# Kernel optimization log

Measured on AMD Instinct MI355X. Metric: run time of the kernel, lower is better.

## Reference

```python
import jax, jax.numpy as jnp
import numpy as np

N_NODES = 100000
N_EDGES = 1200000
NUM_GRAPHS = 128
IN_DIM = 5
HIDDEN = 64


def setup_inputs() -> dict:
    key = jax.random.key(0)
    ks = jax.random.split(key, 12)
    x = jax.random.normal(ks[0], (N_NODES, IN_DIM), dtype=jnp.float32)
    edge_index = jax.random.randint(ks[1], (2, N_EDGES), 0, N_NODES, dtype=jnp.int64 if jax.config.read('jax_enable_x64') else jnp.int32)
    batch = jnp.sort(jax.random.randint(ks[2], (N_NODES,), 0, NUM_GRAPHS, dtype=jnp.int32))
    s = lambda fan_in: 1.0 / np.sqrt(fan_in)
    return {
        'x': x,
        'edge_index': edge_index,
        'batch': batch,
        'w_rel1': jax.random.normal(ks[3], (IN_DIM, HIDDEN), dtype=jnp.float32) * s(IN_DIM),
        'b_rel1': jnp.zeros((HIDDEN,), dtype=jnp.float32),
        'w_root1': jax.random.normal(ks[4], (IN_DIM, HIDDEN), dtype=jnp.float32) * s(IN_DIM),
        'w_rel2': jax.random.normal(ks[5], (HIDDEN, HIDDEN), dtype=jnp.float32) * s(HIDDEN),
        'b_rel2': jnp.zeros((HIDDEN,), dtype=jnp.float32),
        'w_root2': jax.random.normal(ks[6], (HIDDEN, HIDDEN), dtype=jnp.float32) * s(HIDDEN),
        'w_h1': jax.random.normal(ks[7], (2 * HIDDEN, HIDDEN), dtype=jnp.float32) * s(2 * HIDDEN),
        'b_h1': jnp.zeros((HIDDEN,), dtype=jnp.float32),
        'w_h2': jax.random.normal(ks[8], (HIDDEN, 1), dtype=jnp.float32) * s(HIDDEN),
        'b_h2': jnp.zeros((1,), dtype=jnp.float32),
    }


def _graph_conv(x, src, dst, w_rel, b_rel, w_root):
    # PyG GraphConv (aggr='add'): out = aggr(x_src -> dst) @ W_rel + b_rel + x @ W_root
    agg = jax.ops.segment_sum(x[src], dst, num_segments=N_NODES)
    return agg @ w_rel + b_rel + x @ w_root


def reference(x, edge_index, batch,
              w_rel1, b_rel1, w_root1,
              w_rel2, b_rel2, w_root2,
              w_h1, b_h1, w_h2, b_h2):
    src, dst = edge_index[0], edge_index[1]
    h = jax.nn.relu(_graph_conv(x, src, dst, w_rel1, b_rel1, w_root1))
    h = jax.nn.relu(_graph_conv(h, src, dst, w_rel2, b_rel2, w_root2))
    # global add + mean pooling over graphs
    add_pool = jax.ops.segment_sum(h, batch, num_segments=NUM_GRAPHS)
    counts = jax.ops.segment_sum(jnp.ones((N_NODES,), h.dtype), batch, num_segments=NUM_GRAPHS)
    mean_pool = add_pool / jnp.maximum(counts, 1.0)[:, None]
    g = jnp.concatenate([mean_pool, add_pool], axis=1)  # [G, 2*HIDDEN]
    out = jax.nn.relu(g @ w_h1 + b_h1) @ w_h2 + b_h2
    return out.squeeze(-1)
```

## Files before the change

### kernel.cpp

```cpp
#include <hip/hip_runtime.h>
#include <hip/hip_bf16.h>

#define N_NODES    100000
#define N_EDGES    1200000
#define NUM_GRAPHS 128
#define IN_DIM     5
#define HIDDEN     64
#define M_TILES    (N_NODES / 16)
#define NI4        (N_EDGES / 4)

#define CB    782
#define CBLK  256
#define EPB   ((NI4 + CBLK - 1) / CBLK)
#define STCAP 3072
#define AGP   72

typedef __attribute__((ext_vector_type(8))) short short8;
typedef __attribute__((ext_vector_type(4))) float f32x4;
typedef __attribute__((ext_vector_type(2))) float f32x2;

#if defined(__has_builtin)
#if __has_builtin(__builtin_amdgcn_cvt_pk_f32_fp8)
#define HAS_HWF8 1
#endif
#endif

__device__ __forceinline__ unsigned short f2bs(float f) {
    union { float f; unsigned u; } v; v.f = f;
    return (unsigned short)((v.u + 0x7FFFu + ((v.u >> 16) & 1u)) >> 16);
}
__device__ __forceinline__ float bs2f(unsigned short s) {
    union { unsigned u; float f; } v; v.u = ((unsigned)s) << 16;
    return v.f;
}
__device__ __forceinline__ float blo(unsigned p) { return bs2f((unsigned short)(p & 0xffff)); }
__device__ __forceinline__ float bhi(unsigned p) { return bs2f((unsigned short)(p >> 16)); }
__device__ __forceinline__ unsigned pack2(float a, float b) {
    return ((unsigned)f2bs(b) << 16) | (unsigned)f2bs(a);
}

__device__ __forceinline__ unsigned char f2f8(float f) {
    union { float f; unsigned u; } v; v.f = f * 0x1p-120f;
    unsigned u = v.u + 0x7FFFFu + ((v.u >> 20) & 1u);
    return (unsigned char)(u >> 20);
}
__device__ __forceinline__ float f82f(unsigned b) {
    union { unsigned u; float f; } v; v.u = (b & 0x7Fu) << 20;
    return v.f * 0x1p120f;
}

__device__ __forceinline__ void acc8(float4& a, unsigned r) {
#ifdef HAS_HWF8
    f32x2 lo = __builtin_amdgcn_cvt_pk_f32_fp8((int)r, false);
    f32x2 hi = __builtin_amdgcn_cvt_pk_f32_fp8((int)r, true);
    a.x += lo[0]; a.y += lo[1]; a.z += hi[0]; a.w += hi[1];
#else
    a.x += f82f(r); a.y += f82f(r >> 8); a.z += f82f(r >> 16); a.w += f82f(r >> 24);
#endif
}


__global__ void coarse_count(const int* __restrict__ dst, int* __restrict__ gcnt,
                             const float* __restrict__ x, uint4* __restrict__ xb,
                             float* __restrict__ add_pool, int* __restrict__ ptr) {
    __shared__ int h[CB];
    int t = threadIdx.x, b = blockIdx.x;
    for (int i = t; i < CB; i += 256) h[i] = 0;
    __syncthreads();
    int i0 = b * EPB, i1 = min(i0 + EPB, NI4);
    for (int i = i0 + t; i < i1; i += 256) {
        int4 d = ((const int4*)dst)[i];
        atomicAdd(&h[d.x >> 7], 1);
        atomicAdd(&h[d.y >> 7], 1);
        atomicAdd(&h[d.z >> 7], 1);
        atomicAdd(&h[d.w >> 7], 1);
    }
    __syncthreads();
    for (int i = t; i < CB; i += 256) gcnt[b * CB + i] = h[i];

    for (int n = b * 256 + t; n < N_NODES; n += CBLK * 256) {
        const float* xr = x + (size_t)n * IN_DIM;
        uint4 o;
        o.x = pack2(xr[0], xr[1]);
        o.y = pack2(xr[2], xr[3]);
        o.z = pack2(xr[4], 0.0f);
        o.w = 0u;
        xb[n] = o;
    }
    if (b == 0) {
        for (int i = t; i < NUM_GRAPHS * HIDDEN; i += 256) add_pool[i] = 0.0f;
        if (t == 0) ptr[N_NODES] = N_EDGES;
    }
}

__global__ void block_scan(int* __restrict__ gcnt, int* __restrict__ btot) {
    __shared__ int s[CBLK];
    int k = blockIdx.x, t = threadIdx.x;
    int v = gcnt[t * CB + k];
    s[t] = v;
    __syncthreads();
    for (int off = 1; off < CBLK; off <<= 1) {
        int u = (t >= off) ? s[t - off] : 0;
        __syncthreads();
        s[t] += u;
        __syncthreads();
    }
    gcnt[t * CB + k] = s[t] - v;
    if (t == CBLK - 1) btot[k] = s[t];
}

__global__ void partition_k(const int* __restrict__ src, const int* __restrict__ dst,
                            const int* __restrict__ gcnt, const int* __restrict__ btot,
                            int* __restrict__ bstart, int* __restrict__ part) {
    __shared__ int sb[CB];
    __shared__ int base[CB];
    __shared__ int h[CB];
    int t = threadIdx.x, b = blockIdx.x;
    for (int i = t; i < CB; i += 256) sb[i] = btot[i];
    __syncthreads();
    if (t < 64) {
        int loc[13];
        int base_i = t * 13;
        int sum = 0;
#pragma unroll
        for (int j = 0; j < 13; ++j) {
            int idx = base_i + j;
            int c = (idx < CB) ? sb[idx] : 0;
            loc[j] = sum; sum += c;
        }
        int inc = sum;
#pragma unroll
        for (int off = 1; off < 64; off <<= 1) {
            int u = __shfl_up(inc, off, 64);
            if (t >= off) inc += u;
        }
        int excl = inc - sum;
#pragma unroll
        for (int j = 0; j < 13; ++j) {
            int idx = base_i + j;
            if (idx < CB) sb[idx] = excl + loc[j];
        }
    }
    __syncthreads();
    for (int i = t; i < CB; i += 256) {
        int bs = sb[i];
        base[i] = bs + gcnt[b * CB + i];
        h[i] = 0;
        if (b == 0) bstart[i] = bs;
    }
    if (b == 0 && t == 0) bstart[CB] = N_EDGES;
    __syncthreads();
    int i0 = b * EPB, i1 = min(i0 + EPB, NI4);
    for (int i = i0 + t; i < i1; i += 256) {
        int4 s4 = ((const int4*)src)[i];
        int4 d4 = ((const int4*)dst)[i];
        int k, r;
        k = d4.x >> 7; r = atomicAdd(&h[k], 1); part[base[k] + r] = s4.x | ((d4.x & 127) << 17);
        k = d4.y >> 7; r = atomicAdd(&h[k], 1); part[base[k] + r] = s4.y | ((d4.y & 127) << 17);
        k = d4.z >> 7; r = atomicAdd(&h[k], 1); part[base[k] + r] = s4.z | ((d4.z & 127) << 17);
        k = d4.w >> 7; r = atomicAdd(&h[k], 1); part[base[k] + r] = s4.w | ((d4.w & 127) << 17);
    }
}

__global__ void fine_gather1(const int* __restrict__ part, const int* __restrict__ bstart,
                             int* __restrict__ ptr, int* __restrict__ esrc,
                             const uint4* __restrict__ xb,
                             const float* __restrict__ x,
                             const float* __restrict__ w_rel1,
                             const float* __restrict__ b_rel1,
                             const float* __restrict__ w_root1,
                             unsigned short* __restrict__ h1,
                             unsigned char* __restrict__ h1f8) {
    __shared__ int fh[128];
    __shared__ int fo[128];
    __shared__ int fr[128];
    __shared__ uint4 stage[STCAP];
    int k = blockIdx.x, t = threadIdx.x;
    int e0 = bstart[k], e1 = bstart[k + 1];
    int ne = e1 - e0;
    bool useLds = (ne <= STCAP);
    if (t < 128) { fh[t] = 0; fr[t] = 0; }
    __syncthreads();
    for (int e = e0 + t; e < e1; e += 256)
        atomicAdd(&fh[(part[e] >> 17) & 127], 1);
    __syncthreads();
    int v = (t < 128) ? fh[t] : 0;
    if (t < 128) fo[t] = v;
    __syncthreads();
    for (int off = 1; off < 128; off <<= 1) {
        int u = (t >= off && t < 128) ? fo[t - off] : 0;
        __syncthreads();
        if (t < 128) fo[t] += u;
        __syncthreads();
    }
    if (t < 128) {
        int excl = fo[t] - v;
        int n_t = (k << 7) + t;
        if (n_t < N_NODES) ptr[n_t] = e0 + excl;
        fh[t] = excl;
    }
    __syncthreads();
    for (int e = e0 + t; e < e1; e += 256) {
        int p = part[e];
        int d = (p >> 17) & 127;
        int s = p & 0x1FFFF;
        int r = atomicAdd(&fr[d], 1);
        int slot = fh[d] + r;
        esrc[e0 + slot] = s;
        if (useLds) stage[slot] = xb[s];
    }
    __syncthreads();

    int ql = t & 15;
    int g  = t >> 4;
    float wr[IN_DIM][4], wo[IN_DIM][4], bias[4];
#pragma unroll
    for (int j = 0; j < 4; ++j) {
        int ch = ql * 4 + j;
        bias[j] = b_rel1[ch];
#pragma unroll
        for (int kk = 0; kk < IN_DIM; ++kk) {
            wr[kk][j] = w_rel1[kk * HIDDEN + ch];
            wo[kk][j] = w_root1[kk * HIDDEN + ch];
        }
    }

    for (int nl = g; nl < 128; nl += 16) {
        int n = (k << 7) + nl;
        if (n >= N_NODES) break;
        int s0 = fh[nl];
        int s1 = (nl < 127) ? fh[nl + 1] : ne;
        float a[IN_DIM] = {0.f, 0.f, 0.f, 0.f, 0.f};
        if (useLds) {
            for (int i = s0 + ql; i < s1; i += 16) {
                uint4 p = stage[i];
                a[0] += blo(p.x); a[1] += bhi(p.x);
                a[2] += blo(p.y); a[3] += bhi(p.y);
                a[4] += blo(p.z);
            }
        } else {
            for (int i = s0 + ql; i < s1; i += 16) {
                uint4 p = xb[esrc[e0 + i]];
                a[0] += blo(p.x); a[1] += bhi(p.x);
                a[2] += blo(p.y); a[3] += bhi(p.y);
                a[4] += blo(p.z);
            }
        }
#pragma unroll
        for (int kk = 0; kk < IN_DIM; ++kk) {
            a[kk] += __shfl_xor(a[kk], 1, 64);
            a[kk] += __shfl_xor(a[kk], 2, 64);
            a[kk] += __shfl_xor(a[kk], 4, 64);
            a[kk] += __shfl_xor(a[kk], 8, 64);
        }
        float xr[IN_DIM];
#pragma unroll
        for (int kk = 0; kk < IN_DIM; ++kk) xr[kk] = x[(size_t)n * IN_DIM + kk];

        unsigned short hv[4];
        unsigned char  hf[4];
#pragma unroll
        for (int j = 0; j < 4; ++j) {
            float acc = bias[j];
#pragma unroll
            for (int kk = 0; kk < IN_DIM; ++kk)
                acc += a[kk] * wr[kk][j] + xr[kk] * wo[kk][j];
            float h = fmaxf(acc, 0.0f);
            hv[j] = f2bs(h);
            hf[j] = f2f8(h);
        }
        ushort4 v4; v4.x = hv[0]; v4.y = hv[1]; v4.z = hv[2]; v4.w = hv[3];
        *(ushort4*)(h1 + (size_t)n * HIDDEN + ql * 4) = v4;
        uchar4 c4; c4.x = hf[0]; c4.y = hf[1]; c4.z = hf[2]; c4.w = hf[3];
        *(uchar4*)(h1f8 + (size_t)n * HIDDEN + ql * 4) = c4;
    }
}

__global__ void gather2_mlp2(const unsigned* __restrict__ rows,
                             const int* __restrict__ ptr,
                             const int* __restrict__ esrc,
                             const unsigned short* __restrict__ h1,
                             const float* __restrict__ w_rel2,
                             const float* __restrict__ b_rel2,
                             const float* __restrict__ w_root2,
                             const int* __restrict__ batch,
                             float* __restrict__ add_pool) {
    __shared__ unsigned short ag[16 * AGP];
    int tid  = threadIdx.x;
    int lane = tid & 63, wv = tid >> 6;
    int row  = lane & 15, quad = lane >> 4;
    int n    = wv * 16 + row;
    int g    = tid >> 4, ql = tid & 15;

    short8 bwr[2], bwo[2];
#pragma unroll
    for (int s = 0; s < 2; ++s)
#pragma unroll
        for (int j = 0; j < 8; ++j) {
            int k = 32 * s + quad * 8 + j;
            bwr[s][j] = (short)f2bs(w_rel2[k * HIDDEN + n]);
            bwo[s][j] = (short)f2bs(w_root2[k * HIDDEN + n]);
        }
    float bias = b_rel2[n];

    for (int t = blockIdx.x; t < M_TILES; t += gridDim.x) {
        int m0 = t * 16;
        int nd = m0 + g;
        int start = ptr[nd], end = ptr[nd + 1];
        float4 a0 = {0.f, 0.f, 0.f, 0.f}, a1 = a0;
        int e = start;
        for (; e + 1 < end; e += 2) {
            int sA = esrc[e], sB = esrc[e + 1];
            unsigned r0 = rows[(size_t)sA * 16 + ql];
            unsigned r1 = rows[(size_t)sB * 16 + ql];
            acc8(a0, r0); acc8(a1, r1);
        }
        if (e < end) {
            unsigned r0 = rows[(size_t)esrc[e] * 16 + ql];
            acc8(a0, r0);
        }
        a0.x += a1.x; a0.y += a1.y; a0.z += a1.z; a0.w += a1.w;
        uint2 pk;
        pk.x = pack2(a0.x, a0.y);
        pk.y = pack2(a0.z, a0.w);
        *(uint2*)&ag[g * AGP + ql * 4] = pk;
        __syncthreads();

        size_t rbase = (size_t)(m0 + row) * HIDDEN;
        short8 aa0 = *(const short8*)&ag[row * AGP + quad * 8];
        short8 aa1 = *(const short8*)&ag[row * AGP + 32 + quad * 8];
        short8 ah0 = *(const short8*)(h1 + rbase + quad * 8);
        short8 ah1 = *(const short8*)(h1 + rbase + 32 + quad * 8);

        f32x4 acc = {bias, bias, bias, bias};
        acc = __builtin_amdgcn_mfma_f32_16x16x32_bf16(aa0, bwr[0], acc, 0, 0, 0);
        acc = __builtin_amdgcn_mfma_f32_16x16x32_bf16(aa1, bwr[1], acc, 0, 0, 0);
        acc = __builtin_amdgcn_mfma_f32_16x16x32_bf16(ah0, bwo[0], acc, 0, 0, 0);
        acc = __builtin_amdgcn_mfma_f32_16x16x32_bf16(ah1, bwo[1], acc, 0, 0, 0);

        float hv0 = fmaxf(acc[0], 0.0f), hv1 = fmaxf(acc[1], 0.0f);
        float hv2 = fmaxf(acc[2], 0.0f), hv3 = fmaxf(acc[3], 0.0f);

        int gLo = batch[m0], gHi = batch[m0 + 15];
        if (gLo == gHi) {
            float s = (hv0 + hv1) + (hv2 + hv3);
            s += __shfl_xor(s, 16, 64);
            s += __shfl_xor(s, 32, 64);
            if (quad == 0)
                atomicAdd(&add_pool[gLo * HIDDEN + n], s);
        } else {
            int m = m0 + quad * 4;
            atomicAdd(&add_pool[batch[m]     * HIDDEN + n], hv0);
            atomicAdd(&add_pool[batch[m + 1] * HIDDEN + n], hv1);
            atomicAdd(&add_pool[batch[m + 2] * HIDDEN + n], hv2);
            atomicAdd(&add_pool[batch[m + 3] * HIDDEN + n], hv3);
        }
        __syncthreads();
    }
}

__device__ __forceinline__ int lower_bound_i(const int* a, int n, int v) {
    int lo = 0, hi = n;
    while (lo < hi) { int mid = (lo + hi) >> 1; if (a[mid] < v) lo = mid + 1; else hi = mid; }
    return lo;
}

__global__ void head_mlp(const float* __restrict__ add_pool,
                         const int* __restrict__ batch,
                         const float* __restrict__ w_h1,
                         const float* __restrict__ b_h1,
                         const float* __restrict__ w_h2,
                         const float* __restrict__ b_h2,
                         float* __restrict__ out) {
    int g = blockIdx.x, t = threadIdx.x;

    __shared__ int s_cnt;
    if (t == 0) {
        int start = lower_bound_i(batch, N_NODES, g);
        int end   = lower_bound_i(batch, N_NODES, g + 1);
        s_cnt = end - start;
    }
    __syncthreads();
    float cnt = fmaxf((float)s_cnt, 1.0f);

    __shared__ float sg[2 * HIDDEN];
    float add = add_pool[(size_t)g * HIDDEN + t];
    sg[t]          = add / cnt;
    sg[HIDDEN + t] = add;
    __syncthreads();

    float hid = b_h1[t];
#pragma unroll 16
    for (int i = 0; i < 2 * HIDDEN; ++i)
        hid += sg[i] * w_h1[i * HIDDEN + t];
    hid = fmaxf(hid, 0.0f);

    float res = hid * w_h2[t];
    for (int off = 32; off > 0; off >>= 1)
        res += __shfl_down(res, off, 64);
    if (t == 0) out[g] = res + b_h2[0];
}

extern "C" void kernel_launch(void* const* d_in, const int* in_sizes, int n_in,
                              void* d_out, int out_size, void* d_ws, size_t ws_size,
                              hipStream_t stream) {
    const float* x       = (const float*)d_in[0];
    const int*   ei      = (const int*)d_in[1];
    const int*   src     = ei;
    const int*   dst     = ei + N_EDGES;
    const int*   batch   = (const int*)d_in[2];
    const float* w_rel1  = (const float*)d_in[3];
    const float* b_rel1  = (const float*)d_in[4];
    const float* w_root1 = (const float*)d_in[5];
    const float* w_rel2  = (const float*)d_in[6];
    const float* b_rel2  = (const float*)d_in[7];
    const float* w_root2 = (const float*)d_in[8];
    const float* w_h1    = (const float*)d_in[9];
    const float* b_h1    = (const float*)d_in[10];
    const float* w_h2    = (const float*)d_in[11];
    const float* b_h2    = (const float*)d_in[12];
    float* out = (float*)d_out;

    int* base = (int*)d_ws;
    int*   gcnt     = base;
    int*   btot     = gcnt + ((CBLK * CB + 3) & ~3);
    int*   bstart   = btot + ((CB + 3) & ~3);
    float* add_pool = (float*)(bstart + ((CB + 1 + 3) & ~3));
    int*   ptr      = (int*)(add_pool + NUM_GRAPHS * HIDDEN);
    int*   part     = ptr + ((N_NODES + 1 + 3) & ~3);
    int*   esrc     = part + N_EDGES;
    unsigned short* h1   = (unsigned short*)(esrc + N_EDGES);
    unsigned char*  h1f8 = (unsigned char*)(h1 + (size_t)N_NODES * HIDDEN);
    uint4*          xb   = (uint4*)(h1f8 + (size_t)N_NODES * HIDDEN);

    coarse_count<<<CBLK, 256, 0, stream>>>(dst, gcnt, x, xb, add_pool, ptr);
    block_scan<<<CB, CBLK, 0, stream>>>(gcnt, btot);
    partition_k<<<CBLK, 256, 0, stream>>>(src, dst, gcnt, btot, bstart, part);

    fine_gather1<<<CB, 256, 0, stream>>>(part, bstart, ptr, esrc, xb, x,
                                         w_rel1, b_rel1, w_root1, h1, h1f8);
    gather2_mlp2<<<2048, 256, 0, stream>>>((const unsigned*)h1f8, ptr, esrc, h1,
                                           w_rel2, b_rel2, w_root2, batch, add_pool);
    head_mlp<<<NUM_GRAPHS, 64, 0, stream>>>(add_pool, batch, w_h1, b_h1, w_h2, b_h2, out);
}
```

Baseline: 190.3 us.

## Give each wavefront its own 16-node tile in layer-2 gather+MLP, drop LDS staging

```diff
diff --git a/kernel.cpp b/kernel.cpp
--- a/kernel.cpp
+++ b/kernel.cpp
@@ -13,7 +13,6 @@
 #define CBLK  256
 #define EPB   ((NI4 + CBLK - 1) / CBLK)
 #define STCAP 3072
-#define AGP   72
 
 typedef __attribute__((ext_vector_type(8))) short short8;
 typedef __attribute__((ext_vector_type(4))) float f32x4;
@@ -285,77 +284,90 @@
                              const float* __restrict__ w_root2,
                              const int* __restrict__ batch,
                              float* __restrict__ add_pool) {
-    __shared__ unsigned short ag[16 * AGP];
     int tid  = threadIdx.x;
     int lane = tid & 63, wv = tid >> 6;
-    int row  = lane & 15, quad = lane >> 4;
-    int n    = wv * 16 + row;
-    int g    = tid >> 4, ql = tid & 15;
-
-    short8 bwr[2], bwo[2];
-#pragma unroll
-    for (int s = 0; s < 2; ++s)
-#pragma unroll
-        for (int j = 0; j < 8; ++j) {
-            int k = 32 * s + quad * 8 + j;
-            bwr[s][j] = (short)f2bs(w_rel2[k * HIDDEN + n]);
-            bwo[s][j] = (short)f2bs(w_root2[k * HIDDEN + n]);
-        }
-    float bias = b_rel2[n];
-
-    for (int t = blockIdx.x; t < M_TILES; t += gridDim.x) {
+    int r    = lane & 15, quad = lane >> 4;
+
+    short8 bwr[4][2], bwo[4][2];
+    float bias[4];
+#pragma unroll
+    for (int cb = 0; cb < 4; ++cb) {
+        int n = cb * 16 + r;
+        bias[cb] = b_rel2[n];
+#pragma unroll
+        for (int s = 0; s < 2; ++s)
+#pragma unroll
+            for (int j = 0; j < 8; ++j) {
+                int k = 32 * s + quad * 8 + j;
+                bwr[cb][s][j] = (short)f2bs(w_rel2[k * HIDDEN + n]);
+                bwo[cb][s][j] = (short)f2bs(w_root2[k * HIDDEN + n]);
+            }
+    }
+
+    int gw = blockIdx.x * 4 + wv;
+    int nw = gridDim.x * 4;
+    for (int t = gw; t < M_TILES; t += nw) {
         int m0 = t * 16;
-        int nd = m0 + g;
-        int start = ptr[nd], end = ptr[nd + 1];
-        float4 a0 = {0.f, 0.f, 0.f, 0.f}, a1 = a0;
+        int start = ptr[m0 + r], end = ptr[m0 + r + 1];
+        float4 ac0 = {0.f, 0.f, 0.f, 0.f}, ac1 = ac0, ac2 = ac0, ac3 = ac0;
         int e = start;
         for (; e + 1 < end; e += 2) {
-            int sA = esrc[e], sB = esrc[e + 1];
-            unsigned r0 = rows[(size_t)sA * 16 + ql];
-            unsigned r1 = rows[(size_t)sB * 16 + ql];
-            acc8(a0, r0); acc8(a1, r1);
+            int s0 = esrc[e], s1 = esrc[e + 1];
+            const unsigned* p0 = rows + (size_t)s0 * 16 + 2 * quad;
+            const unsigned* p1 = rows + (size_t)s1 * 16 + 2 * quad;
+            uint2 x0 = *(const uint2*)p0;
+            uint2 y0 = *(const uint2*)(p0 + 8);
+            uint2 x1 = *(const uint2*)p1;
+            uint2 y1 = *(const uint2*)(p1 + 8);
+            acc8(ac0, x0.x); acc8(ac1, x0.y); acc8(ac2, y0.x); acc8(ac3, y0.y);
+            acc8(ac0, x1.x); acc8(ac1, x1.y); acc8(ac2, y1.x); acc8(ac3, y1.y);
         }
         if (e < end) {
-            unsigned r0 = rows[(size_t)esrc[e] * 16 + ql];
-            acc8(a0, r0);
-        }
-        a0.x += a1.x; a0.y += a1.y; a0.z += a1.z; a0.w += a1.w;
-        uint2 pk;
-        pk.x = pack2(a0.x, a0.y);
-        pk.y = pack2(a0.z, a0.w);
-        *(uint2*)&ag[g * AGP + ql * 4] = pk;
-        __syncthreads();
-
-        size_t rbase = (size_t)(m0 + row) * HIDDEN;
-        short8 aa0 = *(const short8*)&ag[row * AGP + quad * 8];
-        short8 aa1 = *(const short8*)&ag[row * AGP + 32 + quad * 8];
-        short8 ah0 = *(const short8*)(h1 + rbase + quad * 8);
-        short8 ah1 = *(const short8*)(h1 + rbase + 32 + quad * 8);
-
-        f32x4 acc = {bias, bias, bias, bias};
-        acc = __builtin_amdgcn_mfma_f32_16x16x32_bf16(aa0, bwr[0], acc, 0, 0, 0);
-        acc = __builtin_amdgcn_mfma_f32_16x16x32_bf16(aa1, bwr[1], acc, 0, 0, 0);
-        acc = __builtin_amdgcn_mfma_f32_16x16x32_bf16(ah0, bwo[0], acc, 0, 0, 0);
-        acc = __builtin_amdgcn_mfma_f32_16x16x32_bf16(ah1, bwo[1], acc, 0, 0, 0);
-
-        float hv0 = fmaxf(acc[0], 0.0f), hv1 = fmaxf(acc[1], 0.0f);
-        float hv2 = fmaxf(acc[2], 0.0f), hv3 = fmaxf(acc[3], 0.0f);
+            const unsigned* p0 = rows + (size_t)esrc[e] * 16 + 2 * quad;
+            uint2 x0 = *(const uint2*)p0;
+            uint2 y0 = *(const uint2*)(p0 + 8);
+            acc8(ac0, x0.x); acc8(ac1, x0.y); acc8(ac2, y0.x); acc8(ac3, y0.y);
+        }
+        short8 aa0, aa1;
+        aa0[0] = (short)f2bs(ac0.x); aa0[1] = (short)f2bs(ac0.y);
+        aa0[2] = (short)f2bs(ac0.z); aa0[3] = (short)f2bs(ac0.w);
+        aa0[4] = (short)f2bs(ac1.x); aa0[5] = (short)f2bs(ac1.y);
+        aa0[6] = (short)f2bs(ac1.z); aa0[7] = (short)f2bs(ac1.w);
+        aa1[0] = (short)f2bs(ac2.x); aa1[1] = (short)f2bs(ac2.y);
+        aa1[2] = (short)f2bs(ac2.z); aa1[3] = (short)f2bs(ac2.w);
+        aa1[4] = (short)f2bs(ac3.x); aa1[5] = (short)f2bs(ac3.y);
+        aa1[6] = (short)f2bs(ac3.z); aa1[7] = (short)f2bs(ac3.w);
+
+        size_t rb = (size_t)(m0 + r) * HIDDEN;
+        short8 ah0 = *(const short8*)(h1 + rb + quad * 8);
+        short8 ah1 = *(const short8*)(h1 + rb + 32 + quad * 8);
 
         int gLo = batch[m0], gHi = batch[m0 + 15];
-        if (gLo == gHi) {
-            float s = (hv0 + hv1) + (hv2 + hv3);
-            s += __shfl_xor(s, 16, 64);
-            s += __shfl_xor(s, 32, 64);
-            if (quad == 0)
-                atomicAdd(&add_pool[gLo * HIDDEN + n], s);
-        } else {
-            int m = m0 + quad * 4;
-            atomicAdd(&add_pool[batch[m]     * HIDDEN + n], hv0);
-            atomicAdd(&add_pool[batch[m + 1] * HIDDEN + n], hv1);
-            atomicAdd(&add_pool[batch[m + 2] * HIDDEN + n], hv2);
-            atomicAdd(&add_pool[batch[m + 3] * HIDDEN + n], hv3);
-        }
-        __syncthreads();
+#pragma unroll
+        for (int cb = 0; cb < 4; ++cb) {
+            f32x4 acc = {bias[cb], bias[cb], bias[cb], bias[cb]};
+            acc = __builtin_amdgcn_mfma_f32_16x16x32_bf16(aa0, bwr[cb][0], acc, 0, 0, 0);
+            acc = __builtin_amdgcn_mfma_f32_16x16x32_bf16(aa1, bwr[cb][1], acc, 0, 0, 0);
+            acc = __builtin_amdgcn_mfma_f32_16x16x32_bf16(ah0, bwo[cb][0], acc, 0, 0, 0);
+            acc = __builtin_amdgcn_mfma_f32_16x16x32_bf16(ah1, bwo[cb][1], acc, 0, 0, 0);
+
+            float hv0 = fmaxf(acc[0], 0.0f), hv1 = fmaxf(acc[1], 0.0f);
+            float hv2 = fmaxf(acc[2], 0.0f), hv3 = fmaxf(acc[3], 0.0f);
+            int n = cb * 16 + r;
+            if (gLo == gHi) {
+                float s = (hv0 + hv1) + (hv2 + hv3);
+                s += __shfl_xor(s, 16, 64);
+                s += __shfl_xor(s, 32, 64);
+                if (quad == 0)
+                    atomicAdd(&add_pool[gLo * HIDDEN + n], s);
+            } else {
+                int m = m0 + quad * 4;
+                atomicAdd(&add_pool[batch[m]     * HIDDEN + n], hv0);
+                atomicAdd(&add_pool[batch[m + 1] * HIDDEN + n], hv1);
+                atomicAdd(&add_pool[batch[m + 2] * HIDDEN + n], hv2);
+                atomicAdd(&add_pool[batch[m + 3] * HIDDEN + n], hv3);
+            }
+        }
     }
 }
 
```

Measured after the change: 192.2 us. No clear change (+1.0%).
